# Kernel optimization log

Measured on AMD Instinct MI355X. Metric: run time of the kernel, lower is better.

The kernel has to match this reference:

```python
import jax, jax.numpy as jnp
import numpy as np

N_HEAD, D_EMB, D_MLP, D_HEAD = 12, 768, 3072, 64
LN_EPS = 1e-5


def setup_inputs() -> dict:
    key = jax.random.key(0)
    ks = jax.random.split(key, 12)
    s = 0.02
    return {
        "x": jax.random.normal(ks[0], (2, 4096, D_EMB), dtype=jnp.float32),
        "ln1_g": jnp.ones((D_EMB,), jnp.float32),
        "ln1_b": jnp.zeros((D_EMB,), jnp.float32),
        "wqkv_w": jax.random.normal(ks[1], (D_EMB, 3 * D_EMB), jnp.float32) * s,
        "wo_w": jax.random.normal(ks[2], (D_EMB, D_EMB), jnp.float32) * s,
        "wo_b": jnp.zeros((D_EMB,), jnp.float32),
        "ln2_g": jnp.ones((D_EMB,), jnp.float32),
        "ln2_b": jnp.zeros((D_EMB,), jnp.float32),
        "w1_w": jax.random.normal(ks[3], (D_EMB, D_MLP), jnp.float32) * s,
        "w1_b": jnp.zeros((D_MLP,), jnp.float32),
        "w2_w": jax.random.normal(ks[4], (D_MLP, D_EMB), jnp.float32) * s,
        "w2_b": jnp.zeros((D_EMB,), jnp.float32),
    }


def _layernorm(x, g, b):
    mu = jnp.mean(x, axis=-1, keepdims=True)
    var = jnp.var(x, axis=-1, keepdims=True)
    return (x - mu) * jax.lax.rsqrt(var + LN_EPS) * g + b


def _attn(x, wqkv_w, wo_w, wo_b):
    B, T, d = x.shape
    qkv = x @ wqkv_w  # [B,T,3d]
    q, k, v = jnp.split(qkv, 3, axis=-1)
    q = q.reshape(B, T, N_HEAD, D_HEAD).transpose(0, 2, 1, 3)  # [B,H,T,dh]
    k = k.reshape(B, T, N_HEAD, D_HEAD).transpose(0, 2, 1, 3)
    v = v.reshape(B, T, N_HEAD, D_HEAD).transpose(0, 2, 1, 3)
    A = jnp.einsum('bhqd,bhkd->bhqk', q, k) / np.sqrt(D_HEAD).astype(np.float32)
    mask = jnp.tril(jnp.ones((T, T), dtype=bool))
    A = jnp.where(mask, A, -jnp.inf)
    A = jax.nn.softmax(A - jax.lax.stop_gradient(jnp.max(A, axis=-1, keepdims=True)), axis=-1)
    y = jnp.einsum('bhqk,bhkd->bhqd', A, v)  # [B,H,T,dh]
    y = y.transpose(0, 2, 1, 3).reshape(B, T, d)
    return y @ wo_w + wo_b


def _mlp(x, w1_w, w1_b, w2_w, w2_b):
    h = jax.nn.gelu(x @ w1_w + w1_b, approximate=False)
    return h @ w2_w + w2_b


def reference(x, ln1_g, ln1_b, wqkv_w, wo_w, wo_b, ln2_g, ln2_b, w1_w, w1_b, w2_w, w2_b):
    x = x + _attn(_layernorm(x, ln1_g, ln1_b), wqkv_w, wo_w, wo_b)
    x = x + _mlp(_layernorm(x, ln2_g, ln2_b), w1_w, w1_b, w2_w, w2_b)
    return x
```

## Files before the change

kernel.cpp:

```cpp
#include <hip/hip_runtime.h>

#define T_SEQ 4096
#define D_EMB 768
#define N_HEAD 12
#define D_HEAD 64
#define D_MLP 3072
#define NTOK 8192
#define QSCALE 0.18033688011112043f

typedef __bf16 v8bf __attribute__((ext_vector_type(8)));
typedef float v4f __attribute__((ext_vector_type(4)));
typedef short v4s __attribute__((ext_vector_type(4)));
typedef unsigned v2u __attribute__((ext_vector_type(2)));

template <int N> struct IC { static constexpr int value = N; };

__device__ __forceinline__ unsigned short f2bf(float f) {
    unsigned int u = __float_as_uint(f);
    unsigned int r = (u + 0x7fffu + ((u >> 16) & 1u)) >> 16;
    return (unsigned short)r;
}

__device__ __forceinline__ void g2lds16(const void* g, void* l) {
    __builtin_amdgcn_global_load_lds(
        (const __attribute__((address_space(1))) void*)g,
        (__attribute__((address_space(3))) void*)l, 16, 0, 0);
}

__device__ __forceinline__ float fastrcp(float x) {
#if __has_builtin(__builtin_amdgcn_rcpf)
    return __builtin_amdgcn_rcpf(x);
#else
    return 1.f / x;
#endif
}

__device__ __forceinline__ void pl32swap(unsigned& a, unsigned& b) {
#if __has_builtin(__builtin_amdgcn_permlane32_swap)
    v2u r = __builtin_amdgcn_permlane32_swap(a, b, false, false);
    a = r[0]; b = r[1];
#else
    asm volatile("v_permlane32_swap_b32 %0, %1" : "+v"(a), "+v"(b));
#endif
}
__device__ __forceinline__ void pl16swap(unsigned& a, unsigned& b) {
#if __has_builtin(__builtin_amdgcn_permlane16_swap)
    v2u r = __builtin_amdgcn_permlane16_swap(a, b, false, false);
    a = r[0]; b = r[1];
#else
    asm volatile("v_permlane16_swap_b32 %0, %1" : "+v"(a), "+v"(b));
#endif
}

__device__ __forceinline__ int sg(int r) { return (r ^ (r >> 2)) & 3; }

__global__ void tcast_kernel(const float* __restrict__ in, unsigned short* __restrict__ out,
                             int K, int N) {
    __shared__ float tile[32][33];
    int k0 = blockIdx.y * 32, n0 = blockIdx.x * 32;
    int tx = threadIdx.x, ty = threadIdx.y;
    for (int i = ty; i < 32; i += 8)
        tile[i][tx] = in[(size_t)(k0 + i) * N + n0 + tx];
    __syncthreads();
    for (int i = ty; i < 32; i += 8)
        out[(size_t)(n0 + i) * K + k0 + tx] = f2bf(tile[tx][i]);
}

__global__ void vtrans_kernel(const unsigned short* __restrict__ in,
                              unsigned short* __restrict__ out) {
    __shared__ unsigned short tile[32][33];
    size_t base = (size_t)blockIdx.z * T_SEQ * D_HEAD;
    int t0 = blockIdx.x * 32, d0 = blockIdx.y * 32;
    int tx = threadIdx.x, ty = threadIdx.y;
    for (int i = ty; i < 32; i += 8)
        tile[i][tx] = in[base + (size_t)(t0 + i) * D_HEAD + d0 + tx];
    __syncthreads();
    size_t tbase = base + (size_t)(t0 >> 6) * 4096 + (t0 & 32);
    for (int i = ty; i < 32; i += 8)
        out[tbase + (size_t)(d0 + i) * 64 + tx] = tile[tx][i];
}

__global__ __launch_bounds__(256) void ln_kernel(const float* __restrict__ x,
                                                 const float* __restrict__ g,
                                                 const float* __restrict__ bta,
                                                 unsigned short* __restrict__ out) {
    int row = blockIdx.x;
    const float* xr = x + (size_t)row * D_EMB;
    int tid = threadIdx.x;
    float v[3];
    float s = 0.f, s2 = 0.f;
#pragma unroll
    for (int i = 0; i < 3; i++) {
        v[i] = xr[tid + i * 256];
        s += v[i];
        s2 += v[i] * v[i];
    }
#pragma unroll
    for (int o = 1; o < 64; o <<= 1) {
        s += __shfl_xor(s, o);
        s2 += __shfl_xor(s2, o);
    }
    __shared__ float red[8];
    int wave = tid >> 6, lane = tid & 63;
    if (lane == 0) { red[wave] = s; red[wave + 4] = s2; }
    __syncthreads();
    s = red[0] + red[1] + red[2] + red[3];
    s2 = red[4] + red[5] + red[6] + red[7];
    float mu = s * (1.f / 768.f);
    float var = s2 * (1.f / 768.f) - mu * mu;
    float rstd = rsqrtf(var + 1e-5f);
#pragma unroll
    for (int i = 0; i < 3; i++) {
        int c = tid + i * 256;
        out[(size_t)row * D_EMB + c] = f2bf((v[i] - mu) * rstd * g[c] + bta[c]);
    }
}

template <int EPI, int MT>
__global__ __launch_bounds__(256) void gemm_kernel(
    const unsigned short* __restrict__ A, const unsigned short* __restrict__ Bt, int K,
    int Nt, const float* __restrict__ bias, const float* __restrict__ resid,
    float* __restrict__ outF, unsigned short* __restrict__ outB,
    unsigned short* __restrict__ Qb, unsigned short* __restrict__ Kb,
    unsigned short* __restrict__ Vb) {
    constexpr int NAI = (MT == 128) ? 4 : 2;
    __shared__ unsigned short As[2][MT * 32];
    __shared__ unsigned short Bs[2][4096];
    const int tid = threadIdx.x;
    const int wave = tid >> 6, lane = tid & 63;
    const int n16 = lane & 15, kq = lane >> 4;
    const int moff = (wave >> 1) * (MT / 2), noff = (wave & 1) * 64;
    const int id = blockIdx.x;
    const int xcd = id & 7, s = id >> 3;
    const int mt = xcd * (NTOK / MT / 8) + s / Nt, nt_ = s % Nt;
    const long m0 = (long)mt * MT, nb0 = (long)nt_ * 128;

    const int c0 = (wave * 2 + 0) * 64 + lane;
    const int c1 = (wave * 2 + 1) * 64 + lane;
    const int r0 = c0 >> 2, r1 = c1 >> 2;
    const unsigned short* bP0 = Bt + (nb0 + r0) * K + (((c0 & 3) ^ sg(r0)) << 3);
    const unsigned short* bP1 = Bt + (nb0 + r1) * K + (((c1 & 3) ^ sg(r1)) << 3);
    const int ca = (MT == 128) ? c0 : (wave * 64 + lane);
    const int ra = ca >> 2;
    const unsigned short* aP0 = A + (m0 + ra) * K + (((ca & 3) ^ sg(ra)) << 3);
    const unsigned short* aP1 = (MT == 128)
        ? A + (m0 + r1) * K + (((c1 & 3) ^ sg(r1)) << 3) : nullptr;
    const int sn = sg(n16);
    const int fw = (noff + n16) * 32 + ((kq ^ sn) << 3);
    const int fa = (moff + n16) * 32 + ((kq ^ sn) << 3);

    const v4f vzero = {0.f, 0.f, 0.f, 0.f};
    v4f acc[4][NAI];
#pragma unroll
    for (int wi = 0; wi < 4; wi++)
#pragma unroll
        for (int ai = 0; ai < NAI; ai++) acc[wi][ai] = vzero;

    auto stage = [&](auto BUFC, int kpos) {
        constexpr int nb = decltype(BUFC)::value;
        if (MT == 128) {
            g2lds16(aP0 + kpos, &As[nb][(wave * 2 + 0) * 512]);
            g2lds16(aP1 + kpos, &As[nb][(wave * 2 + 1) * 512]);
        } else {
            g2lds16(aP0 + kpos, &As[nb][wave * 512]);
        }
        g2lds16(bP0 + kpos, &Bs[nb][(wave * 2 + 0) * 512]);
        g2lds16(bP1 + kpos, &Bs[nb][(wave * 2 + 1) * 512]);
    };
    auto gstep = [&](auto BUFC, int kpos, bool pref) {
        constexpr int buf = decltype(BUFC)::value;
        __syncthreads();
        if (pref) stage(IC<buf ^ 1>{}, kpos + 32);
        v8bf wf[4], af[NAI];
#pragma unroll
        for (int i = 0; i < 4; i++) wf[i] = *(const v8bf*)(&Bs[buf][fw + i * 512]);
#pragma unroll
        for (int i = 0; i < NAI; i++) af[i] = *(const v8bf*)(&As[buf][fa + i * 512]);
#pragma unroll
        for (int wi = 0; wi < 4; wi++)
#pragma unroll
            for (int ai = 0; ai < NAI; ai++)
                acc[wi][ai] = __builtin_amdgcn_mfma_f32_16x16x32_bf16(wf[wi], af[ai],
                                                                     acc[wi][ai], 0, 0, 0);
    };

    stage(IC<0>{}, 0);
#pragma unroll 1
    for (int k0 = 0; k0 < K; k0 += 64) {
        gstep(IC<0>{}, k0, true);
        gstep(IC<1>{}, k0 + 32, k0 + 64 < K);
    }

#pragma unroll
    for (int wi = 0; wi < 4; wi++) {
#pragma unroll
        for (int ai = 0; ai < NAI; ai++) {
            const long Nb = nb0 + noff + wi * 16 + kq * 4;
            const long M = m0 + moff + ai * 16 + n16;
            if (EPI == 0) {
                int which = (int)(Nb / 768);
                int c = (int)(Nb - which * 768);
                int hh = c >> 6, ii = c & 63;
                int bb = (int)(M >> 12), t = (int)(M & 4095);
                size_t dst = (((size_t)bb * N_HEAD + hh) * T_SEQ + t) * D_HEAD + ii;
                union { uint2 u2; unsigned short us[4]; } pk;
#pragma unroll
                for (int r = 0; r < 4; r++) {
                    float v = acc[wi][ai][r];
                    if (which == 0) v *= QSCALE;
                    pk.us[r] = f2bf(v);
                }
                if (which == 0) *(uint2*)(&Qb[dst]) = pk.u2;
                else if (which == 1) *(uint2*)(&Kb[dst]) = pk.u2;
                else *(uint2*)(&Vb[dst]) = pk.u2;
            } else if (EPI == 1) {
                float4 b4 = *(const float4*)(&bias[Nb]);
                float4 r4 = *(const float4*)(&resid[M * 768 + Nb]);
                float4 o4;
                o4.x = acc[wi][ai][0] + b4.x + r4.x;
                o4.y = acc[wi][ai][1] + b4.y + r4.y;
                o4.z = acc[wi][ai][2] + b4.z + r4.z;
                o4.w = acc[wi][ai][3] + b4.w + r4.w;
                *(float4*)(&outF[M * 768 + Nb]) = o4;
            } else {
                float4 b4 = *(const float4*)(&bias[Nb]);
                union { uint2 u2; unsigned short us[4]; } pk;
#pragma unroll
                for (int r = 0; r < 4; r++) {
                    float t = acc[wi][ai][r] + ((const float*)&b4)[r];
                    float y = t * (-2.302118131f + t * t * -0.1029433585f);
                    float gl = t * fastrcp(1.f + __builtin_amdgcn_exp2f(y));
                    pk.us[r] = f2bf(gl);
                }
                *(uint2*)(&outB[M * 3072 + Nb]) = pk.u2;
            }
        }
    }
}

__global__ __launch_bounds__(512, 4) void gemm_splitk_kernel(
    const unsigned short* __restrict__ A, const unsigned short* __restrict__ Bt, int K,
    int Nt, const float* __restrict__ bias, const float* __restrict__ resid,
    float* __restrict__ outF) {
    __shared__ __align__(16) unsigned short SH[32768];
    const int tid = threadIdx.x;
    const int wave = tid >> 6, lane = tid & 63;
    const int kg = wave >> 2, wv = wave & 3;
    const int n16 = lane & 15, kq = lane >> 4;
    const int moff = (wv >> 1) * 64, noff = (wv & 1) * 64;
    const int id = blockIdx.x;
    const int xcd = id & 7, s = id >> 3;
    const int mt = xcd * (NTOK / 128 / 8) + s / Nt, nt_ = s % Nt;
    const long m0 = (long)mt * 128, nb0 = (long)nt_ * 128;
    const int Kh = K >> 1;

    const int c0 = (wv * 2 + 0) * 64 + lane;
    const int c1 = (wv * 2 + 1) * 64 + lane;
    const int r0 = c0 >> 2, r1 = c1 >> 2;
    const int kb = kg * Kh;
    const unsigned short* bP0 = Bt + (nb0 + r0) * K + ((((c0 & 3) ^ sg(r0)) << 3) + kb);
    const unsigned short* bP1 = Bt + (nb0 + r1) * K + ((((c1 & 3) ^ sg(r1)) << 3) + kb);
    const unsigned short* aP0 = A + (m0 + r0) * K + ((((c0 & 3) ^ sg(r0)) << 3) + kb);
    const unsigned short* aP1 = A + (m0 + r1) * K + ((((c1 & 3) ^ sg(r1)) << 3) + kb);
    const int sn = sg(n16);
    const int fw = (noff + n16) * 32 + ((kq ^ sn) << 3);
    const int fa = (moff + n16) * 32 + ((kq ^ sn) << 3);
    const int abase = kg * 8192, bbase = 16384 + kg * 8192;

    const v4f vzero = {0.f, 0.f, 0.f, 0.f};
    v4f acc[4][4];
#pragma unroll
    for (int wi = 0; wi < 4; wi++)
#pragma unroll
        for (int ai = 0; ai < 4; ai++) acc[wi][ai] = vzero;

    auto stage = [&](auto BUFC, int kpos) {
        constexpr int nb = decltype(BUFC)::value;
        unsigned short* asb = SH + abase + nb * 4096;
        unsigned short* bsb = SH + bbase + nb * 4096;
        g2lds16(aP0 + kpos, asb + (wv * 2 + 0) * 512);
        g2lds16(aP1 + kpos, asb + (wv * 2 + 1) * 512);
        g2lds16(bP0 + kpos, bsb + (wv * 2 + 0) * 512);
        g2lds16(bP1 + kpos, bsb + (wv * 2 + 1) * 512);
    };
    auto gstep = [&](auto BUFC, int kpos, bool pref) {
        constexpr int buf = decltype(BUFC)::value;
        __syncthreads();
        if (pref) stage(IC<buf ^ 1>{}, kpos + 32);
        const unsigned short* asb = SH + abase + buf * 4096;
        const unsigned short* bsb = SH + bbase + buf * 4096;
        v8bf wf[4], af[4];
#pragma unroll
        for (int i = 0; i < 4; i++) wf[i] = *(const v8bf*)(bsb + fw + i * 512);
#pragma unroll
        for (int i = 0; i < 4; i++) af[i] = *(const v8bf*)(asb + fa + i * 512);
#pragma unroll
        for (int wi = 0; wi < 4; wi++)
#pragma unroll
            for (int ai = 0; ai < 4; ai++)
                acc[wi][ai] = __builtin_amdgcn_mfma_f32_16x16x32_bf16(wf[wi], af[ai],
                                                                     acc[wi][ai], 0, 0, 0);
    };

    stage(IC<0>{}, 0);
#pragma unroll 1
    for (int k0 = 0; k0 < Kh; k0 += 64) {
        gstep(IC<0>{}, k0, true);
        gstep(IC<1>{}, k0 + 32, k0 + 64 < Kh);
    }

    __syncthreads();
    v4f* ex = (v4f*)SH;
    if (kg == 1) {
#pragma unroll
        for (int wi = 0; wi < 4; wi++)
#pragma unroll
            for (int ai = 0; ai < 4; ai++)
                ex[((wv * 16 + wi * 4 + ai) << 6) + lane] = acc[wi][ai];
    }
    __syncthreads();
    if (kg == 1) return;

#pragma unroll
    for (int wi = 0; wi < 4; wi++) {
#pragma unroll
        for (int ai = 0; ai < 4; ai++) {
            v4f p = ex[((wv * 16 + wi * 4 + ai) << 6) + lane];
            const long Nb = nb0 + noff + wi * 16 + kq * 4;
            const long M = m0 + moff + ai * 16 + n16;
            float4 b4 = *(const float4*)(&bias[Nb]);
            float4 r4 = *(const float4*)(&resid[M * 768 + Nb]);
            float4 o4;
            o4.x = acc[wi][ai][0] + p[0] + b4.x + r4.x;
            o4.y = acc[wi][ai][1] + p[1] + b4.y + r4.y;
            o4.z = acc[wi][ai][2] + p[2] + b4.z + r4.z;
            o4.w = acc[wi][ai][3] + p[3] + b4.w + r4.w;
            *(float4*)(&outF[M * 768 + Nb]) = o4;
        }
    }
}

__global__ __launch_bounds__(512) void attn_kernel(const unsigned short* __restrict__ Q,
                                                   const unsigned short* __restrict__ Kg,
                                                   const unsigned short* __restrict__ Vt,
                                                   unsigned short* __restrict__ y) {
    __shared__ unsigned short Kt[2][4096];
    __shared__ unsigned short Vl[2][4096];
    const int tid = threadIdx.x;
    const int wave = tid >> 6, lane = tid & 63;
    const int n16 = lane & 15, kq = lane >> 4;
    const int id = blockIdx.x;
    const int xcd = id & 7, slot = id >> 3;
    const int combo = xcd * 3 + (slot % 3);
    const int qt2 = 31 - slot / 3;
    const int h = combo % N_HEAD, b = combo / N_HEAD;
    const size_t hoff = (((size_t)b * N_HEAD + h) * T_SEQ) * D_HEAD;
    const unsigned short* Qh = Q + hoff;
    const unsigned short* Kh = Kg + hoff;
    const unsigned short* Vh = Vt + hoff;
    const v4f vzero = {0.f, 0.f, 0.f, 0.f};

    const int sC = wave * 64 + lane;
    const int soff = (sC >> 3) * 64 + ((((sC & 7) ^ ((sC >> 3) & 7))) << 3);
    const int fb0 = n16 * 64 + ((kq ^ (n16 & 7)) << 3);
    const int fb1 = n16 * 64 + (((4 + kq) ^ (n16 & 7)) << 3);
    v8bf vone;
#pragma unroll
    for (int j = 0; j < 8; j++) ((unsigned short*)&vone)[j] = 0x3F80;

    const int qglob = qt2 * 128 + wave * 16 + n16;
    v8bf qf[2];
#pragma unroll
    for (int ks = 0; ks < 2; ks++)
        qf[ks] = *(const v8bf*)(&Qh[(size_t)qglob * D_HEAD + ks * 32 + kq * 8]);

    v4f o[4], lacc;
#pragma unroll
    for (int nt = 0; nt < 4; nt++) o[nt] = vzero;
    lacc = vzero;

    const unsigned short* knext;
    const unsigned short* vnext;

    auto step = [&](auto BUFC, int kt, bool pref, bool diag) {
        constexpr int buf = decltype(BUFC)::value;
        __syncthreads();
        if (pref) {
            g2lds16(knext + soff, &Kt[buf ^ 1][wave * 512]);
            g2lds16(vnext + soff, &Vl[buf ^ 1][wave * 512]);
            knext += 4096;
            vnext += 4096;
        }
        v4f s[4];
#pragma unroll
        for (int nt = 0; nt < 4; nt++) s[nt] = vzero;
        __builtin_amdgcn_s_setprio(1);
#pragma unroll
        for (int nt = 0; nt < 4; nt++) {
            v8bf k0 = *(const v8bf*)(&Kt[buf][nt * 1024 + fb0]);
            v8bf k1 = *(const v8bf*)(&Kt[buf][nt * 1024 + fb1]);
            s[nt] = __builtin_amdgcn_mfma_f32_16x16x32_bf16(k0, qf[0], s[nt], 0, 0, 0);
            s[nt] = __builtin_amdgcn_mfma_f32_16x16x32_bf16(k1, qf[1], s[nt], 0, 0, 0);
        }
        __builtin_amdgcn_s_setprio(0);
        union PW { v4s s4; unsigned u[2]; } pa[4];
#pragma unroll
        for (int ntk = 0; ntk < 4; ntk++) {
            union { v4s s4; __bf16 h[4]; } pk;
#pragma unroll
            for (int r = 0; r < 4; r++) {
                float p = __builtin_amdgcn_exp2f(s[ntk][r]);
                if (diag) {
                    int key = kt * 64 + ntk * 16 + kq * 4 + r;
                    if (key > qglob) p = 0.f;
                }
                pk.h[r] = (__bf16)p;
            }
            pa[ntk].s4 = pk.s4;
        }
        union F8 { v8bf v; unsigned u[4]; } pf[2];
#pragma unroll
        for (int ks = 0; ks < 2; ks++) {
#pragma unroll
            for (int j = 0; j < 2; j++) {
                unsigned X = pa[2 * ks].u[j], Y = pa[2 * ks + 1].u[j];
                pl32swap(X, Y);
                pl16swap(X, Y);
                pf[ks].u[j] = X;
                pf[ks].u[j + 2] = Y;
            }
        }
        __builtin_amdgcn_s_setprio(1);
#pragma unroll
        for (int ks = 0; ks < 2; ks++) {
            lacc = __builtin_amdgcn_mfma_f32_16x16x32_bf16(pf[ks].v, vone, lacc, 0, 0, 0);
#pragma unroll
            for (int nt = 0; nt < 4; nt++) {
                v8bf vb = *(const v8bf*)(&Vl[buf][nt * 1024 + (ks ? fb1 : fb0)]);
                o[nt] = __builtin_amdgcn_mfma_f32_16x16x32_bf16(pf[ks].v, vb, o[nt], 0, 0, 0);
            }
        }
        __builtin_amdgcn_s_setprio(0);
    };

    g2lds16(Kh + soff, &Kt[0][wave * 512]);
    g2lds16(Vh + soff, &Vl[0][wave * 512]);
    knext = Kh + 4096;
    vnext = Vh + 4096;

    const int nst = 2 * qt2 + 2;
    int kt = 0;
#pragma unroll 1
    while (kt < nst - 2) {
        step(IC<0>{}, kt, true, false);
        step(IC<1>{}, kt + 1, true, false);
        kt += 2;
    }
    step(IC<0>{}, kt, true, true);
    step(IC<1>{}, kt + 1, false, true);

    float linv[4];
#pragma unroll
    for (int r = 0; r < 4; r++) linv[r] = fastrcp(lacc[r]);
#pragma unroll
    for (int nt = 0; nt < 4; nt++)
#pragma unroll
        for (int r = 0; r < 4; r++) {
            int q = qt2 * 128 + wave * 16 + kq * 4 + r;
            float val = o[nt][r] * linv[r];
            y[((size_t)b * T_SEQ + q) * D_EMB + h * 64 + nt * 16 + n16] = f2bf(val);
        }
}

extern "C" void kernel_launch(void* const* d_in, const int* in_sizes, int n_in,
                              void* d_out, int out_size, void* d_ws, size_t ws_size,
                              hipStream_t stream) {
    const float* x = (const float*)d_in[0];
    const float* ln1_g = (const float*)d_in[1];
    const float* ln1_b = (const float*)d_in[2];
    const float* wqkv_w = (const float*)d_in[3];
    const float* wo_w = (const float*)d_in[4];
    const float* wo_b = (const float*)d_in[5];
    const float* ln2_g = (const float*)d_in[6];
    const float* ln2_b = (const float*)d_in[7];
    const float* w1_w = (const float*)d_in[8];
    const float* w1_b = (const float*)d_in[9];
    const float* w2_w = (const float*)d_in[10];
    const float* w2_b = (const float*)d_in[11];
    float* out = (float*)d_out;

    char* ws = (char*)d_ws;
    size_t off = 0;
    auto alloc = [&](size_t bytes) -> void* {
        void* p = ws + off;
        off += (bytes + 255) & ~(size_t)255;
        return p;
    };
    unsigned short* xn = (unsigned short*)alloc((size_t)NTOK * D_EMB * 2);
    unsigned short* wqkvT = (unsigned short*)alloc((size_t)2304 * 768 * 2);
    unsigned short* woT = (unsigned short*)alloc((size_t)768 * 768 * 2);
    unsigned short* w1T = (unsigned short*)alloc((size_t)3072 * 768 * 2);
    unsigned short* w2T = (unsigned short*)alloc((size_t)768 * 3072 * 2);
    unsigned short* Qb = (unsigned short*)alloc((size_t)NTOK * D_EMB * 2);
    unsigned short* Kb = (unsigned short*)alloc((size_t)NTOK * D_EMB * 2);
    unsigned short* Vb = (unsigned short*)alloc((size_t)NTOK * D_EMB * 2);
    unsigned short* yb = (unsigned short*)alloc((size_t)NTOK * D_EMB * 2);
    float* res1 = (float*)alloc((size_t)NTOK * D_EMB * 4);
    unsigned short* Vtb = xn;
    unsigned short* hbuf = Qb;

    dim3 tb(32, 8);
    tcast_kernel<<<dim3(2304 / 32, 768 / 32), tb, 0, stream>>>(wqkv_w, wqkvT, 768, 2304);
    tcast_kernel<<<dim3(768 / 32, 768 / 32), tb, 0, stream>>>(wo_w, woT, 768, 768);
    tcast_kernel<<<dim3(3072 / 32, 768 / 32), tb, 0, stream>>>(w1_w, w1T, 768, 3072);
    tcast_kernel<<<dim3(768 / 32, 3072 / 32), tb, 0, stream>>>(w2_w, w2T, 3072, 768);

    ln_kernel<<<NTOK, 256, 0, stream>>>(x, ln1_g, ln1_b, xn);

    gemm_kernel<0, 128><<<1152, 256, 0, stream>>>(
        xn, wqkvT, 768, 18, nullptr, nullptr, nullptr, nullptr, Qb, Kb, Vb);

    vtrans_kernel<<<dim3(T_SEQ / 32, 2, 2 * N_HEAD), tb, 0, stream>>>(Vb, Vtb);

    attn_kernel<<<768, 512, 0, stream>>>(Qb, Kb, Vtb, yb);

    gemm_splitk_kernel<<<384, 512, 0, stream>>>(
        yb, woT, 768, 6, wo_b, x, res1);

    ln_kernel<<<NTOK, 256, 0, stream>>>(res1, ln2_g, ln2_b, xn);

    gemm_kernel<2, 128><<<1536, 256, 0, stream>>>(
        xn, w1T, 768, 24, w1_b, nullptr, nullptr, hbuf, nullptr, nullptr, nullptr);

    gemm_splitk_kernel<<<384, 512, 0, stream>>>(
        hbuf, w2T, 3072, 6, w2_b, res1, out);
}
```

Measured before the change: 404.0 us.

## Widen QKV and W1 GEMM tiles to 128x256 with 512-thread blocks

Replaces the 128x128, 256-thread GEMM used for the QKV and first MLP projections with a 128x256 tile computed by 8 waves in a 2x4 arrangement. Each block reuses its A tile across twice as many output columns, which cuts global and LDS traffic for A and halves the number of blocks. In exchange it uses more LDS per block (48 KB) and a launch-bounds hint of 6 blocks per CU, which may limit occupancy or force register spills, and the smaller grids (576 and 768 blocks) may load the CUs less evenly. The unused residual epilogue path is removed.

```diff
diff --git a/kernel.cpp b/kernel.cpp
--- a/kernel.cpp
+++ b/kernel.cpp
@@ -116,70 +116,58 @@
     }
 }
 
-template <int EPI, int MT>
-__global__ __launch_bounds__(256) void gemm_kernel(
+template <int EPI>
+__global__ __launch_bounds__(512, 6) void gemm_wide_kernel(
     const unsigned short* __restrict__ A, const unsigned short* __restrict__ Bt, int K,
-    int Nt, const float* __restrict__ bias, const float* __restrict__ resid,
-    float* __restrict__ outF, unsigned short* __restrict__ outB,
+    int Nt, const float* __restrict__ bias, unsigned short* __restrict__ outB,
     unsigned short* __restrict__ Qb, unsigned short* __restrict__ Kb,
     unsigned short* __restrict__ Vb) {
-    constexpr int NAI = (MT == 128) ? 4 : 2;
-    __shared__ unsigned short As[2][MT * 32];
-    __shared__ unsigned short Bs[2][4096];
+    __shared__ unsigned short As[2][4096];
+    __shared__ unsigned short Bs[2][8192];
     const int tid = threadIdx.x;
     const int wave = tid >> 6, lane = tid & 63;
     const int n16 = lane & 15, kq = lane >> 4;
-    const int moff = (wave >> 1) * (MT / 2), noff = (wave & 1) * 64;
+    const int moff = (wave >> 2) * 64, noff = (wave & 3) * 64;
     const int id = blockIdx.x;
     const int xcd = id & 7, s = id >> 3;
-    const int mt = xcd * (NTOK / MT / 8) + s / Nt, nt_ = s % Nt;
-    const long m0 = (long)mt * MT, nb0 = (long)nt_ * 128;
-
-    const int c0 = (wave * 2 + 0) * 64 + lane;
-    const int c1 = (wave * 2 + 1) * 64 + lane;
-    const int r0 = c0 >> 2, r1 = c1 >> 2;
-    const unsigned short* bP0 = Bt + (nb0 + r0) * K + (((c0 & 3) ^ sg(r0)) << 3);
-    const unsigned short* bP1 = Bt + (nb0 + r1) * K + (((c1 & 3) ^ sg(r1)) << 3);
-    const int ca = (MT == 128) ? c0 : (wave * 64 + lane);
-    const int ra = ca >> 2;
-    const unsigned short* aP0 = A + (m0 + ra) * K + (((ca & 3) ^ sg(ra)) << 3);
-    const unsigned short* aP1 = (MT == 128)
-        ? A + (m0 + r1) * K + (((c1 & 3) ^ sg(r1)) << 3) : nullptr;
+    const int mt = xcd * 8 + s / Nt, nt_ = s % Nt;
+    const long m0 = (long)mt * 128, nb0 = (long)nt_ * 256;
+
+    const int rA = tid >> 2;
+    const unsigned short* aP = A + (m0 + rA) * K + (((tid & 3) ^ sg(rA)) << 3);
+    const unsigned short* bP0 = Bt + (nb0 + rA) * K + (((tid & 3) ^ sg(rA)) << 3);
+    const int cB1 = tid + 512, rB1 = cB1 >> 2;
+    const unsigned short* bP1 = Bt + (nb0 + rB1) * K + (((cB1 & 3) ^ sg(rB1)) << 3);
     const int sn = sg(n16);
     const int fw = (noff + n16) * 32 + ((kq ^ sn) << 3);
     const int fa = (moff + n16) * 32 + ((kq ^ sn) << 3);
 
     const v4f vzero = {0.f, 0.f, 0.f, 0.f};
-    v4f acc[4][NAI];
+    v4f acc[4][4];
 #pragma unroll
     for (int wi = 0; wi < 4; wi++)
 #pragma unroll
-        for (int ai = 0; ai < NAI; ai++) acc[wi][ai] = vzero;
+        for (int ai = 0; ai < 4; ai++) acc[wi][ai] = vzero;
 
     auto stage = [&](auto BUFC, int kpos) {
         constexpr int nb = decltype(BUFC)::value;
-        if (MT == 128) {
-            g2lds16(aP0 + kpos, &As[nb][(wave * 2 + 0) * 512]);
-            g2lds16(aP1 + kpos, &As[nb][(wave * 2 + 1) * 512]);
-        } else {
-            g2lds16(aP0 + kpos, &As[nb][wave * 512]);
-        }
-        g2lds16(bP0 + kpos, &Bs[nb][(wave * 2 + 0) * 512]);
-        g2lds16(bP1 + kpos, &Bs[nb][(wave * 2 + 1) * 512]);
+        g2lds16(aP + kpos, &As[nb][wave * 512]);
+        g2lds16(bP0 + kpos, &Bs[nb][wave * 512]);
+        g2lds16(bP1 + kpos, &Bs[nb][4096 + wave * 512]);
     };
     auto gstep = [&](auto BUFC, int kpos, bool pref) {
         constexpr int buf = decltype(BUFC)::value;
         __syncthreads();
         if (pref) stage(IC<buf ^ 1>{}, kpos + 32);
-        v8bf wf[4], af[NAI];
+        v8bf wf[4], af[4];
 #pragma unroll
         for (int i = 0; i < 4; i++) wf[i] = *(const v8bf*)(&Bs[buf][fw + i * 512]);
 #pragma unroll
-        for (int i = 0; i < NAI; i++) af[i] = *(const v8bf*)(&As[buf][fa + i * 512]);
+        for (int i = 0; i < 4; i++) af[i] = *(const v8bf*)(&As[buf][fa + i * 512]);
 #pragma unroll
         for (int wi = 0; wi < 4; wi++)
 #pragma unroll
-            for (int ai = 0; ai < NAI; ai++)
+            for (int ai = 0; ai < 4; ai++)
                 acc[wi][ai] = __builtin_amdgcn_mfma_f32_16x16x32_bf16(wf[wi], af[ai],
                                                                      acc[wi][ai], 0, 0, 0);
     };
@@ -194,7 +182,7 @@
 #pragma unroll
     for (int wi = 0; wi < 4; wi++) {
 #pragma unroll
-        for (int ai = 0; ai < NAI; ai++) {
+        for (int ai = 0; ai < 4; ai++) {
             const long Nb = nb0 + noff + wi * 16 + kq * 4;
             const long M = m0 + moff + ai * 16 + n16;
             if (EPI == 0) {
@@ -213,15 +201,6 @@
                 if (which == 0) *(uint2*)(&Qb[dst]) = pk.u2;
                 else if (which == 1) *(uint2*)(&Kb[dst]) = pk.u2;
                 else *(uint2*)(&Vb[dst]) = pk.u2;
-            } else if (EPI == 1) {
-                float4 b4 = *(const float4*)(&bias[Nb]);
-                float4 r4 = *(const float4*)(&resid[M * 768 + Nb]);
-                float4 o4;
-                o4.x = acc[wi][ai][0] + b4.x + r4.x;
-                o4.y = acc[wi][ai][1] + b4.y + r4.y;
-                o4.z = acc[wi][ai][2] + b4.z + r4.z;
-                o4.w = acc[wi][ai][3] + b4.w + r4.w;
-                *(float4*)(&outF[M * 768 + Nb]) = o4;
             } else {
                 float4 b4 = *(const float4*)(&bias[Nb]);
                 union { uint2 u2; unsigned short us[4]; } pk;
@@ -517,8 +496,8 @@
 
     ln_kernel<<<NTOK, 256, 0, stream>>>(x, ln1_g, ln1_b, xn);
 
-    gemm_kernel<0, 128><<<1152, 256, 0, stream>>>(
-        xn, wqkvT, 768, 18, nullptr, nullptr, nullptr, nullptr, Qb, Kb, Vb);
+    gemm_wide_kernel<0><<<576, 512, 0, stream>>>(
+        xn, wqkvT, 768, 9, nullptr, nullptr, Qb, Kb, Vb);
 
     vtrans_kernel<<<dim3(T_SEQ / 32, 2, 2 * N_HEAD), tb, 0, stream>>>(Vb, Vtb);
 
@@ -529,8 +508,8 @@
 
     ln_kernel<<<NTOK, 256, 0, stream>>>(res1, ln2_g, ln2_b, xn);
 
-    gemm_kernel<2, 128><<<1536, 256, 0, stream>>>(
-        xn, w1T, 768, 24, w1_b, nullptr, nullptr, hbuf, nullptr, nullptr, nullptr);
+    gemm_wide_kernel<2><<<768, 512, 0, stream>>>(
+        xn, w1T, 768, 12, w1_b, hbuf, nullptr, nullptr, nullptr);
 
     gemm_splitk_kernel<<<384, 512, 0, stream>>>(
         hbuf, w2T, 3072, 6, w2_b, res1, out);
```

After: 655.7 us. 62.3% more time.

## Fuse V transpose into QKV GEMM epilogue, merge weight casts into one launch

Applied to the files above, without the earlier changes.

The V head transpose now happens inside the QKV projection epilogue, so the separate vtrans kernel is gone and V is written straight into the tiled layout attention expects. The QKV GEMM moves from the 256-thread kernel to the 512-thread split-K kernel, and the four weight transpose-cast launches become a single kernel. This removes one full pass over V plus launch overhead. In exchange, V is written with scattered 2-byte stores, and the split-K QKV path adds an LDS reduction.

```diff
diff --git a/kernel.cpp b/kernel.cpp
--- a/kernel.cpp
+++ b/kernel.cpp
@@ -54,30 +54,25 @@
 
 __device__ __forceinline__ int sg(int r) { return (r ^ (r >> 2)) & 3; }
 
-__global__ void tcast_kernel(const float* __restrict__ in, unsigned short* __restrict__ out,
-                             int K, int N) {
+__global__ void tcast4_kernel(const float* __restrict__ i0, unsigned short* __restrict__ o0,
+                              const float* __restrict__ i1, unsigned short* __restrict__ o1,
+                              const float* __restrict__ i2, unsigned short* __restrict__ o2,
+                              const float* __restrict__ i3, unsigned short* __restrict__ o3) {
     __shared__ float tile[32][33];
-    int k0 = blockIdx.y * 32, n0 = blockIdx.x * 32;
+    int id = blockIdx.x;
+    const float* in; unsigned short* out; int K, N, t;
+    if (id < 1728)      { in = i0; out = o0; K = 768;  N = 2304; t = id; }
+    else if (id < 2304) { in = i1; out = o1; K = 768;  N = 768;  t = id - 1728; }
+    else if (id < 4608) { in = i2; out = o2; K = 768;  N = 3072; t = id - 2304; }
+    else                { in = i3; out = o3; K = 3072; N = 768;  t = id - 4608; }
+    int nw = N / 32;
+    int n0 = (t % nw) * 32, k0 = (t / nw) * 32;
     int tx = threadIdx.x, ty = threadIdx.y;
     for (int i = ty; i < 32; i += 8)
         tile[i][tx] = in[(size_t)(k0 + i) * N + n0 + tx];
     __syncthreads();
     for (int i = ty; i < 32; i += 8)
         out[(size_t)(n0 + i) * K + k0 + tx] = f2bf(tile[tx][i]);
-}
-
-__global__ void vtrans_kernel(const unsigned short* __restrict__ in,
-                              unsigned short* __restrict__ out) {
-    __shared__ unsigned short tile[32][33];
-    size_t base = (size_t)blockIdx.z * T_SEQ * D_HEAD;
-    int t0 = blockIdx.x * 32, d0 = blockIdx.y * 32;
-    int tx = threadIdx.x, ty = threadIdx.y;
-    for (int i = ty; i < 32; i += 8)
-        tile[i][tx] = in[base + (size_t)(t0 + i) * D_HEAD + d0 + tx];
-    __syncthreads();
-    size_t tbase = base + (size_t)(t0 >> 6) * 4096 + (t0 & 32);
-    for (int i = ty; i < 32; i += 8)
-        out[tbase + (size_t)(d0 + i) * 64 + tx] = tile[tx][i];
 }
 
 __global__ __launch_bounds__(256) void ln_kernel(const float* __restrict__ x,
@@ -119,11 +114,8 @@
 template <int EPI, int MT>
 __global__ __launch_bounds__(256) void gemm_kernel(
     const unsigned short* __restrict__ A, const unsigned short* __restrict__ Bt, int K,
-    int Nt, const float* __restrict__ bias, const float* __restrict__ resid,
-    float* __restrict__ outF, unsigned short* __restrict__ outB,
-    unsigned short* __restrict__ Qb, unsigned short* __restrict__ Kb,
-    unsigned short* __restrict__ Vb) {
-    constexpr int NAI = (MT == 128) ? 4 : 2;
+    int Nt, const float* __restrict__ bias, unsigned short* __restrict__ outB) {
+    constexpr int NAI = 4;
     __shared__ unsigned short As[2][MT * 32];
     __shared__ unsigned short Bs[2][4096];
     const int tid = threadIdx.x;
@@ -140,11 +132,8 @@
     const int r0 = c0 >> 2, r1 = c1 >> 2;
     const unsigned short* bP0 = Bt + (nb0 + r0) * K + (((c0 & 3) ^ sg(r0)) << 3);
     const unsigned short* bP1 = Bt + (nb0 + r1) * K + (((c1 & 3) ^ sg(r1)) << 3);
-    const int ca = (MT == 128) ? c0 : (wave * 64 + lane);
-    const int ra = ca >> 2;
-    const unsigned short* aP0 = A + (m0 + ra) * K + (((ca & 3) ^ sg(ra)) << 3);
-    const unsigned short* aP1 = (MT == 128)
-        ? A + (m0 + r1) * K + (((c1 & 3) ^ sg(r1)) << 3) : nullptr;
+    const unsigned short* aP0 = A + (m0 + r0) * K + (((c0 & 3) ^ sg(r0)) << 3);
+    const unsigned short* aP1 = A + (m0 + r1) * K + (((c1 & 3) ^ sg(r1)) << 3);
     const int sn = sg(n16);
     const int fw = (noff + n16) * 32 + ((kq ^ sn) << 3);
     const int fa = (moff + n16) * 32 + ((kq ^ sn) << 3);
@@ -158,12 +147,8 @@
 
     auto stage = [&](auto BUFC, int kpos) {
         constexpr int nb = decltype(BUFC)::value;
-        if (MT == 128) {
-            g2lds16(aP0 + kpos, &As[nb][(wave * 2 + 0) * 512]);
-            g2lds16(aP1 + kpos, &As[nb][(wave * 2 + 1) * 512]);
-        } else {
-            g2lds16(aP0 + kpos, &As[nb][wave * 512]);
-        }
+        g2lds16(aP0 + kpos, &As[nb][(wave * 2 + 0) * 512]);
+        g2lds16(aP1 + kpos, &As[nb][(wave * 2 + 1) * 512]);
         g2lds16(bP0 + kpos, &Bs[nb][(wave * 2 + 0) * 512]);
         g2lds16(bP1 + kpos, &Bs[nb][(wave * 2 + 1) * 512]);
     };
@@ -197,51 +182,26 @@
         for (int ai = 0; ai < NAI; ai++) {
             const long Nb = nb0 + noff + wi * 16 + kq * 4;
             const long M = m0 + moff + ai * 16 + n16;
-            if (EPI == 0) {
-                int which = (int)(Nb / 768);
-                int c = (int)(Nb - which * 768);
-                int hh = c >> 6, ii = c & 63;
-                int bb = (int)(M >> 12), t = (int)(M & 4095);
-                size_t dst = (((size_t)bb * N_HEAD + hh) * T_SEQ + t) * D_HEAD + ii;
-                union { uint2 u2; unsigned short us[4]; } pk;
-#pragma unroll
-                for (int r = 0; r < 4; r++) {
-                    float v = acc[wi][ai][r];
-                    if (which == 0) v *= QSCALE;
-                    pk.us[r] = f2bf(v);
-                }
-                if (which == 0) *(uint2*)(&Qb[dst]) = pk.u2;
-                else if (which == 1) *(uint2*)(&Kb[dst]) = pk.u2;
-                else *(uint2*)(&Vb[dst]) = pk.u2;
-            } else if (EPI == 1) {
-                float4 b4 = *(const float4*)(&bias[Nb]);
-                float4 r4 = *(const float4*)(&resid[M * 768 + Nb]);
-                float4 o4;
-                o4.x = acc[wi][ai][0] + b4.x + r4.x;
-                o4.y = acc[wi][ai][1] + b4.y + r4.y;
-                o4.z = acc[wi][ai][2] + b4.z + r4.z;
-                o4.w = acc[wi][ai][3] + b4.w + r4.w;
-                *(float4*)(&outF[M * 768 + Nb]) = o4;
-            } else {
-                float4 b4 = *(const float4*)(&bias[Nb]);
-                union { uint2 u2; unsigned short us[4]; } pk;
-#pragma unroll
-                for (int r = 0; r < 4; r++) {
-                    float t = acc[wi][ai][r] + ((const float*)&b4)[r];
-                    float y = t * (-2.302118131f + t * t * -0.1029433585f);
-                    float gl = t * fastrcp(1.f + __builtin_amdgcn_exp2f(y));
-                    pk.us[r] = f2bf(gl);
-                }
-                *(uint2*)(&outB[M * 3072 + Nb]) = pk.u2;
+            float4 b4 = *(const float4*)(&bias[Nb]);
+            union { uint2 u2; unsigned short us[4]; } pk;
+#pragma unroll
+            for (int r = 0; r < 4; r++) {
+                float t = acc[wi][ai][r] + ((const float*)&b4)[r];
+                float y = t * (-2.302118131f + t * t * -0.1029433585f);
+                float gl = t * fastrcp(1.f + __builtin_amdgcn_exp2f(y));
+                pk.us[r] = f2bf(gl);
             }
-        }
-    }
-}
-
+            *(uint2*)(&outB[M * 3072 + Nb]) = pk.u2;
+        }
+    }
+}
+
+template <int EPI>
 __global__ __launch_bounds__(512, 4) void gemm_splitk_kernel(
     const unsigned short* __restrict__ A, const unsigned short* __restrict__ Bt, int K,
     int Nt, const float* __restrict__ bias, const float* __restrict__ resid,
-    float* __restrict__ outF) {
+    float* __restrict__ outF, unsigned short* __restrict__ Qb,
+    unsigned short* __restrict__ Kb, unsigned short* __restrict__ Vb) {
     __shared__ __align__(16) unsigned short SH[32768];
     const int tid = threadIdx.x;
     const int wave = tid >> 6, lane = tid & 63;
@@ -250,7 +210,7 @@
     const int moff = (wv >> 1) * 64, noff = (wv & 1) * 64;
     const int id = blockIdx.x;
     const int xcd = id & 7, s = id >> 3;
-    const int mt = xcd * (NTOK / 128 / 8) + s / Nt, nt_ = s % Nt;
+    const int mt = xcd * 8 + s / Nt, nt_ = s % Nt;
     const long m0 = (long)mt * 128, nb0 = (long)nt_ * 128;
     const int Kh = K >> 1;
 
@@ -328,14 +288,40 @@
             v4f p = ex[((wv * 16 + wi * 4 + ai) << 6) + lane];
             const long Nb = nb0 + noff + wi * 16 + kq * 4;
             const long M = m0 + moff + ai * 16 + n16;
-            float4 b4 = *(const float4*)(&bias[Nb]);
-            float4 r4 = *(const float4*)(&resid[M * 768 + Nb]);
-            float4 o4;
-            o4.x = acc[wi][ai][0] + p[0] + b4.x + r4.x;
-            o4.y = acc[wi][ai][1] + p[1] + b4.y + r4.y;
-            o4.z = acc[wi][ai][2] + p[2] + b4.z + r4.z;
-            o4.w = acc[wi][ai][3] + p[3] + b4.w + r4.w;
-            *(float4*)(&outF[M * 768 + Nb]) = o4;
+            if (EPI == 0) {
+                int which = (int)(Nb / 768);
+                int c = (int)(Nb - which * 768);
+                int hh = c >> 6, ii = c & 63;
+                int bb = (int)(M >> 12), t = (int)(M & 4095);
+                if (which == 2) {
+                    size_t basev = ((size_t)bb * N_HEAD + hh) * T_SEQ * D_HEAD;
+                    size_t dstv = basev + (size_t)(t >> 6) * 4096 +
+                                  (size_t)ii * 64 + (t & 63);
+#pragma unroll
+                    for (int r = 0; r < 4; r++)
+                        Vb[dstv + r * 64] = f2bf(acc[wi][ai][r] + p[r]);
+                } else {
+                    size_t dst = (((size_t)bb * N_HEAD + hh) * T_SEQ + t) * D_HEAD + ii;
+                    union { uint2 u2; unsigned short us[4]; } pk;
+#pragma unroll
+                    for (int r = 0; r < 4; r++) {
+                        float v = acc[wi][ai][r] + p[r];
+                        if (which == 0) v *= QSCALE;
+                        pk.us[r] = f2bf(v);
+                    }
+                    if (which == 0) *(uint2*)(&Qb[dst]) = pk.u2;
+                    else *(uint2*)(&Kb[dst]) = pk.u2;
+                }
+            } else {
+                float4 b4 = *(const float4*)(&bias[Nb]);
+                float4 r4 = *(const float4*)(&resid[M * 768 + Nb]);
+                float4 o4;
+                o4.x = acc[wi][ai][0] + p[0] + b4.x + r4.x;
+                o4.y = acc[wi][ai][1] + p[1] + b4.y + r4.y;
+                o4.z = acc[wi][ai][2] + p[2] + b4.z + r4.z;
+                o4.w = acc[wi][ai][3] + p[3] + b4.w + r4.w;
+                *(float4*)(&outF[M * 768 + Nb]) = o4;
+            }
         }
     }
 }
@@ -506,32 +492,27 @@
     unsigned short* Vb = (unsigned short*)alloc((size_t)NTOK * D_EMB * 2);
     unsigned short* yb = (unsigned short*)alloc((size_t)NTOK * D_EMB * 2);
     float* res1 = (float*)alloc((size_t)NTOK * D_EMB * 4);
-    unsigned short* Vtb = xn;
     unsigned short* hbuf = Qb;
 
     dim3 tb(32, 8);
-    tcast_kernel<<<dim3(2304 / 32, 768 / 32), tb, 0, stream>>>(wqkv_w, wqkvT, 768, 2304);
-    tcast_kernel<<<dim3(768 / 32, 768 / 32), tb, 0, stream>>>(wo_w, woT, 768, 768);
-    tcast_kernel<<<dim3(3072 / 32, 768 / 32), tb, 0, stream>>>(w1_w, w1T, 768, 3072);
-    tcast_kernel<<<dim3(768 / 32, 3072 / 32), tb, 0, stream>>>(w2_w, w2T, 3072, 768);
+    tcast4_kernel<<<6912, tb, 0, stream>>>(wqkv_w, wqkvT, wo_w, woT,
+                                           w1_w, w1T, w2_w, w2T);
 
     ln_kernel<<<NTOK, 256, 0, stream>>>(x, ln1_g, ln1_b, xn);
 
-    gemm_kernel<0, 128><<<1152, 256, 0, stream>>>(
-        xn, wqkvT, 768, 18, nullptr, nullptr, nullptr, nullptr, Qb, Kb, Vb);
-
-    vtrans_kernel<<<dim3(T_SEQ / 32, 2, 2 * N_HEAD), tb, 0, stream>>>(Vb, Vtb);
-
-    attn_kernel<<<768, 512, 0, stream>>>(Qb, Kb, Vtb, yb);
-
-    gemm_splitk_kernel<<<384, 512, 0, stream>>>(
-        yb, woT, 768, 6, wo_b, x, res1);
+    gemm_splitk_kernel<0><<<1152, 512, 0, stream>>>(
+        xn, wqkvT, 768, 18, nullptr, nullptr, nullptr, Qb, Kb, Vb);
+
+    attn_kernel<<<768, 512, 0, stream>>>(Qb, Kb, Vb, yb);
+
+    gemm_splitk_kernel<1><<<384, 512, 0, stream>>>(
+        yb, woT, 768, 6, wo_b, x, res1, nullptr, nullptr, nullptr);
 
     ln_kernel<<<NTOK, 256, 0, stream>>>(res1, ln2_g, ln2_b, xn);
 
     gemm_kernel<2, 128><<<1536, 256, 0, stream>>>(
-        xn, w1T, 768, 24, w1_b, nullptr, nullptr, hbuf, nullptr, nullptr, nullptr);
-
-    gemm_splitk_kernel<<<384, 512, 0, stream>>>(
-        hbuf, w2T, 3072, 6, w2_b, res1, out);
-}
+        xn, w1T, 768, 24, w1_b, hbuf);
+
+    gemm_splitk_kernel<1><<<384, 512, 0, stream>>>(
+        hbuf, w2T, 3072, 6, w2_b, res1, out, nullptr, nullptr, nullptr);
+}
```

Result: faster. 395.1 us (-2.2%).
